# Optimization experiments

Hardware: AMD Instinct MI355X
Metric: run time of the kernel (lower is better)

The kernel has to match this reference:

```python
import jax, jax.numpy as jnp
import numpy as np

B, S, D, H = 4, 1024, 1024, 16
HD = D // H  # per-head dim = 64
NEG = -10000000000.0


def setup_inputs() -> dict:
    key = jax.random.key(0)
    ks = jax.random.split(key, 12)
    q = jax.random.normal(ks[0], (B, S, D), jnp.float32)
    k = jax.random.normal(ks[1], (B, S, D), jnp.float32)
    v = jax.random.normal(ks[2], (B, S, D), jnp.float32)
    mask = jax.random.randint(ks[3], (B, S, S), 0, 2).astype(jnp.int32)
    sc = 1.0 / np.sqrt(D)
    Wq = jax.random.normal(ks[4], (H, D, HD), jnp.float32) * sc
    bq = jnp.zeros((H, HD), jnp.float32)
    Wk = jax.random.normal(ks[5], (H, D, HD), jnp.float32) * sc
    bk = jnp.zeros((H, HD), jnp.float32)
    Wv = jax.random.normal(ks[6], (H, D, HD), jnp.float32) * sc
    bv = jnp.zeros((H, HD), jnp.float32)
    Wo = jax.random.normal(ks[7], (D, D), jnp.float32) * sc
    bo = jnp.zeros((D,), jnp.float32)
    return {"query": q, "key": k, "value": v, "attention_mask": mask,
            "Wq": Wq, "bq": bq, "Wk": Wk, "bk": bk, "Wv": Wv, "bv": bv,
            "Wo": Wo, "bo": bo}


def reference(query, key, value, attention_mask, Wq, bq, Wk, bk, Wv, bv, Wo, bo):
    # batched per-head projections: [B,S,D] x [H,D,E] -> [B,H,S,E]
    q = jnp.einsum('bsd,hde->bhse', query, Wq) + bq[None, :, None, :]
    k = jnp.einsum('bsd,hde->bhse', key, Wk) + bk[None, :, None, :]
    v = jnp.einsum('bsd,hde->bhse', value, Wv) + bv[None, :, None, :]
    # NOTE: scale uses key_dim (model_size = full D), faithful to source
    score = jnp.einsum('bhse,bhte->bhst', q, k) / jnp.sqrt(jnp.float32(D))
    m = attention_mask.astype(jnp.float32)[:, None, :, :]  # [B,1,S,S]
    score = score + (1.0 - m) * NEG
    attn = jax.nn.softmax(score, axis=-1) * m  # double masking
    heads = jnp.einsum('bhst,bhte->bhse', attn, v)  # [B,H,S,E]
    # concat heads along feature dim (head order preserved)
    heads = heads.transpose(0, 2, 1, 3).reshape(B, S, D)
    return heads @ Wo + bo
```

## Files before the change

kernel.cpp:

```cpp
#include <hip/hip_runtime.h>

#define B_ 4
#define S_ 1024
#define D_ 1024
#define H_ 16
#define E_ 64
#define BS_ (B_*S_)
#define BHSE_ (B_*H_*S_*E_)

typedef __attribute__((ext_vector_type(8))) short bf16x8;
typedef __attribute__((ext_vector_type(4))) float f32x4;

__device__ __forceinline__ unsigned short f2bf(float f) {
    unsigned int x = __float_as_uint(f);
    x = (x + 0x7FFFu + ((x >> 16) & 1u)) >> 16;
    return (unsigned short)x;
}
__device__ __forceinline__ float bf2f(unsigned short u) {
    return __uint_as_float(((unsigned int)u) << 16);
}
__device__ __forceinline__ float ldin(const void* p, size_t i, int isb) {
    return isb ? bf2f(((const unsigned short*)p)[i]) : ((const float*)p)[i];
}

#if __has_builtin(__builtin_amdgcn_exp2f)
#define EXP2(x) __builtin_amdgcn_exp2f(x)
#else
#define EXP2(x) __expf((x) * 0.6931471805599453f)
#endif

__device__ __forceinline__ void gl2lds16(const void* g, void* l) {
    __builtin_amdgcn_global_load_lds(
        (const __attribute__((address_space(1))) void*)g,
        (__attribute__((address_space(3))) void*)l, 16, 0, 0);
}

__global__ void detect_dtype(const unsigned int* q, int* flag) {
    __shared__ int cnt;
    if (threadIdx.x == 0) cnt = 0;
    __syncthreads();
    unsigned int w = q[threadIdx.x];
    unsigned int lo = w & 0xFFFFu;
    unsigned int e = (lo >> 7) & 0xFFu;
    int ok = (lo == 0u) || (e >= 100u && e <= 145u);
    atomicAdd(&cnt, ok);
    __syncthreads();
    if (threadIdx.x == 0) flag[0] = (cnt >= 240) ? 1 : 0;
}

__global__ __launch_bounds__(256) void conv_w2(
        const void* Wq, const void* Wk, const void* Wv, const void* Wo,
        const void* bq_, const void* bk_, const void* bv_, const void* bo_,
        unsigned short* WT, float* biases, const int* flag) {
    __shared__ unsigned short Tt[64][72];
    const int isb = flag[0];
    const int z = blockIdx.z, t = threadIdx.x;
    const void* src = (z == 0) ? Wq : (z == 1) ? Wk : (z == 2) ? Wv : Wo;
    const int r0 = blockIdx.y * 64;
    const int c0 = blockIdx.x;
    {
        int dl = t >> 2, qc = t & 3;
        size_t base;
        if (z < 3) base = (size_t)c0 * 65536 + (size_t)(r0 + dl) * 64 + qc * 16;
        else       base = (size_t)(r0 + dl) * 1024 + (size_t)c0 * 64 + qc * 16;
        if (isb) {
            const unsigned short* s = (const unsigned short*)src + base;
            bf16x8 a0 = *(const bf16x8*)s, a1 = *(const bf16x8*)(s + 8);
#pragma unroll
            for (int j = 0; j < 8; j++) {
                Tt[qc * 16 + j][dl] = (unsigned short)a0[j];
                Tt[qc * 16 + 8 + j][dl] = (unsigned short)a1[j];
            }
        } else {
            const float* s = (const float*)src + base;
#pragma unroll
            for (int j = 0; j < 16; j++) Tt[qc * 16 + j][dl] = f2bf(s[j]);
        }
    }
    __syncthreads();
    {
        int el = t >> 2, qc = t & 3;
        size_t dst = (size_t)z * D_ * D_ + (size_t)(c0 * 64 + el) * D_ + r0 + qc * 16;
        *(bf16x8*)&WT[dst]     = *(const bf16x8*)&Tt[el][qc * 16];
        *(bf16x8*)&WT[dst + 8] = *(const bf16x8*)&Tt[el][qc * 16 + 8];
    }
    if (z == 3 && blockIdx.y == 0 && blockIdx.x < 4) {
        const void* bs = (blockIdx.x == 0) ? bq_ : (blockIdx.x == 1) ? bk_
                       : (blockIdx.x == 2) ? bv_ : bo_;
#pragma unroll
        for (int j = 0; j < 4; j++) {
            int i = t * 4 + j;
            biases[blockIdx.x * 1024 + i] = ldin(bs, i, isb);
        }
    }
}

__global__ void maskpack(const int* mask, unsigned long long* packT) {
    int W = blockIdx.x * 4 + (threadIdx.x >> 6);
    int lane = threadIdx.x & 63;
    int b = W >> 14, rem = W & 16383, s = rem >> 4, kt = rem & 15;
    int mv = mask[((size_t)b * 1024 + s) * 1024 + kt * 64 + lane];
    unsigned long long bits = __ballot(mv != 0);
    if (lane == 0) packT[((size_t)b * 16 + kt) * 1024 + s] = bits;
}

__global__ __launch_bounds__(256) void conv_a(
        const float* q, const float* k, const float* v,
        unsigned short* dst, const int* flag) {
    if (flag[0]) return;
    const int z = blockIdx.x >> 11;
    const float* s = (z == 0) ? q : (z == 1) ? k : v;
    const size_t i = ((size_t)(blockIdx.x & 2047) * 256 + threadIdx.x) * 8;
    f32x4 a0 = *(const f32x4*)(s + i);
    f32x4 a1 = *(const f32x4*)(s + i + 4);
    bf16x8 o;
#pragma unroll
    for (int j = 0; j < 4; j++) {
        o[j]     = (short)f2bf(a0[j]);
        o[4 + j] = (short)f2bf(a1[j]);
    }
    *(bf16x8*)&dst[(size_t)z * ((size_t)BS_ * D_) + i] = o;
}

template<int BM, int BN, int MODE, int MINW>
__global__ __launch_bounds__(256, MINW) void gemm_k(
        const void* A0, const void* A1, const void* A2, const unsigned short* Aconv,
        const unsigned short* BtB, const float* biasB, void* dstB, const int* flag) {
    constexpr int TOT16 = (BM + BN) * 32;
    constexpr int CALLS = TOT16 / 512;
    constexpr int CPW = CALLS / 4;
    constexpr int MT = BM / 32;
    constexpr int NT = BN / 32;
    __shared__ unsigned short buf[2][TOT16];

    const int t = threadIdx.x, lane = t & 63, w = t >> 6;
    const int lm = lane & 15, q4 = lane >> 4;
    const int wm = w >> 1, wn = w & 1;
    const int lr = lane >> 2;
    const int ls = lane & 3;
    const int lg = ls ^ ((lr >> 1) & 3);
    const int fl = flag[0];

    const unsigned short* Abf;
    const unsigned short* Bt;
    const float* bias;
    int z = 0, m0, n0, phase;
    if (MODE == 0) {
        int bid = blockIdx.x + (blockIdx.y << 5) + (blockIdx.z << 9);
        int xcd = bid & 7, idx = bid >> 3;
        z = idx >> 6;
        int r = idx & 63;
        int mt = (xcd << 2) + (r & 3);
        int nt = r >> 2;
        m0 = mt * BM; n0 = nt * BN;
        phase = (nt * 13 + z * 5) & 31;
        const void* Ain = (z == 0) ? A0 : (z == 1 ? A1 : A2);
        Abf = fl ? (const unsigned short*)Ain
                 : Aconv + (size_t)z * ((size_t)BS_ * D_);
        Bt = BtB + (size_t)z * D_ * D_;
        bias = biasB + z * 1024;
    } else {
        Abf = (const unsigned short*)A0;
        Bt = BtB; bias = biasB;
        m0 = blockIdx.x * BM; n0 = blockIdx.y * BN;
        phase = (blockIdx.x * 7 + blockIdx.y * 13) & 31;
    }

    auto stage = [&](int kk, int bi) {
#pragma unroll
        for (int i = 0; i < CPW; ++i) {
            int c = w * CPW + i;
            int row = c * 16 + lr;
            const unsigned short* g;
            if (row < BM)
                g = Abf + (size_t)(m0 + row) * D_ + kk + lg * 8;
            else
                g = Bt + (size_t)(n0 + row - BM) * D_ + kk + lg * 8;
            gl2lds16(g, &buf[bi][c * 512]);
        }
    };

    f32x4 acc[MT][NT];
#pragma unroll
    for (int i = 0; i < MT; i++)
#pragma unroll
        for (int j = 0; j < NT; j++) acc[i][j] = (f32x4){0.f, 0.f, 0.f, 0.f};

    stage((phase & 31) * 32, 0);
    for (int it = 0; it < D_ / 32; ++it) {
        const int bi = it & 1;
        __syncthreads();
        if (it < D_ / 32 - 1) stage(((it + 1 + phase) & 31) * 32, bi ^ 1);

        const unsigned short* As = buf[bi];
        const unsigned short* Bs = buf[bi] + BM * 32;
        bf16x8 af[MT], bv[NT];
#pragma unroll
        for (int mt = 0; mt < MT; mt++) {
            int row = wm * (BM / 2) + mt * 16 + lm;
            af[mt] = *(const bf16x8*)&As[row * 32 + (q4 ^ ((row >> 1) & 3)) * 8];
        }
#pragma unroll
        for (int nt = 0; nt < NT; nt++) {
            int row = wn * (BN / 2) + nt * 16 + lm;
            bv[nt] = *(const bf16x8*)&Bs[row * 32 + (q4 ^ ((row >> 1) & 3)) * 8];
        }
#pragma unroll
        for (int mt = 0; mt < MT; mt++)
#pragma unroll
            for (int nt = 0; nt < NT; nt++)
                acc[mt][nt] = __builtin_amdgcn_mfma_f32_16x16x32_bf16(
                    af[mt], bv[nt], acc[mt][nt], 0, 0, 0);
    }

#pragma unroll
    for (int mt = 0; mt < MT; mt++)
#pragma unroll
        for (int nt = 0; nt < NT; nt++) {
            int N = n0 + wn * (BN / 2) + nt * 16 + lm;
            int Mb = m0 + wm * (BM / 2) + mt * 16 + q4 * 4;
            if (MODE == 0 && z == 2) {
                int bb = Mb >> 10, sb = Mb & 1023, hh = N >> 6, e = N & 63;
                unsigned long long hv = 0;
#pragma unroll
                for (int r = 0; r < 4; r++)
                    hv |= (unsigned long long)f2bf(acc[mt][nt][r] + bias[N]) << (16 * r);
                unsigned short* d16 = (unsigned short*)dstB + (size_t)2 * BHSE_;
                *(unsigned long long*)&d16[(((size_t)(bb * H_ + hh) * E_ + e) << 10) + sb] = hv;
            } else {
#pragma unroll
                for (int r = 0; r < 4; r++) {
                    int M = Mb + r;
                    float v = acc[mt][nt][r] + bias[N];
                    if (MODE == 0) {
                        int bb = M >> 10, s = M & 1023, hh = N >> 6, e = N & 63;
                        unsigned short* d16 = (unsigned short*)dstB + (size_t)z * BHSE_;
                        d16[((size_t)(bb * H_ + hh) * S_ + s) * E_ + e] = f2bf(v);
                    } else {
                        size_t idx = (size_t)M * D_ + N;
                        if (fl) ((unsigned short*)dstB)[idx] = f2bf(v);
                        else    ((float*)dstB)[idx] = v;
                    }
                }
            }
        }
}

#define PSTR 88
__global__ __launch_bounds__(256) void attn64(
        const unsigned short* Qp, const unsigned short* Kp, const unsigned short* VpT,
        const unsigned long long* packT, unsigned short* heads) {
    __shared__ unsigned short KT[2][4096];
    __shared__ unsigned short VT[2][4096];
    __shared__ unsigned short Pw[4][16 * PSTR];

    const int qt = blockIdx.x, h = blockIdx.y, b = blockIdx.z;
    const int t = threadIdx.x, w = t >> 6, lane = t & 63, lm = lane & 15, q4 = lane >> 4;
    const size_t bh = ((size_t)b * H_ + h) * S_ * E_;
    const unsigned short* Qb = Qp + bh;
    const unsigned short* Kb = Kp + bh;
    const unsigned short* Vb = VpT + bh;
    const int q0 = qt * 64 + w * 16;
    unsigned short* P = &Pw[w][0];

    const int l3 = lane >> 3, l7 = lane & 7;
    const int kLaneOff = l3 * 64 + (l7 ^ l3) * 8;
    const int vLaneOff = l3 * 1024 + (l7 ^ l3) * 8;

    const int sw = lm & 7;
    const int c0 = (q4 ^ sw) * 8, c1 = ((q4 ^ 4) ^ sw) * 8;

    bf16x8 bq0 = *(const bf16x8*)&Qb[(size_t)(q0 + lm) * E_ + q4 * 8];
    bf16x8 bq1 = *(const bf16x8*)&Qb[(size_t)(q0 + lm) * E_ + 32 + q4 * 8];

    f32x4 oacc[4];
#pragma unroll
    for (int i = 0; i < 4; i++) oacc[i] = (f32x4){0.f, 0.f, 0.f, 0.f};
    float mrun = -3.0e38f, lrun = 0.f;
    const float scale2 = 0.03125f * 1.4426950408889634f;

#define STAGE(ktile, bufi)                                                    \
    {                                                                         \
        int k0s = (ktile) * 64;                                               \
        _Pragma("unroll")                                                     \
        for (int i_ = 0; i_ < 4; ++i_) {                                      \
            int c_ = w * 4 + i_;                                              \
            if (c_ < 8) {                                                     \
                gl2lds16(Kb + (size_t)k0s * 64 + c_ * 512 + kLaneOff,         \
                         &KT[bufi][c_ * 512]);                                \
            } else {                                                          \
                int cc_ = c_ - 8;                                             \
                gl2lds16(Vb + (size_t)cc_ * 8192 + k0s + vLaneOff,            \
                         &VT[bufi][cc_ * 512]);                               \
            }                                                                 \
        }                                                                     \
    }

    STAGE(0, 0)

    for (int kt = 0; kt < S_ / 64; ++kt) {
        const int bufi = kt & 1;
        __syncthreads();
        if (kt < 15) STAGE(kt + 1, bufi ^ 1)

        unsigned long long mk = packT[((size_t)b * 16 + kt) * 1024 + q0 + lm];

        f32x4 st[4];
#pragma unroll
        for (int jt = 0; jt < 4; ++jt) {
            const unsigned short* kr = &KT[bufi][(jt * 16 + lm) * 64];
            bf16x8 ka0 = *(const bf16x8*)&kr[c0];
            bf16x8 ka1 = *(const bf16x8*)&kr[c1];
            f32x4 zz = (f32x4){0.f, 0.f, 0.f, 0.f};
            zz = __builtin_amdgcn_mfma_f32_16x16x32_bf16(ka0, bq0, zz, 0, 0, 0);
            zz = __builtin_amdgcn_mfma_f32_16x16x32_bf16(ka1, bq1, zz, 0, 0, 0);
            st[jt] = zz;
        }
        float sv[4][4];
        float tmx = -3.0e38f;
#pragma unroll
        for (int jt = 0; jt < 4; ++jt)
#pragma unroll
            for (int r = 0; r < 4; r++) {
                int kb = jt * 16 + q4 * 4 + r;
                float xm = ((mk >> kb) & 1ull) ? st[jt][r] * scale2 : -3.0e38f;
                sv[jt][r] = xm;
                tmx = fmaxf(tmx, xm);
            }
        tmx = fmaxf(tmx, __shfl_xor(tmx, 16, 64));
        tmx = fmaxf(tmx, __shfl_xor(tmx, 32, 64));
        float mnew = fmaxf(mrun, tmx);
        float alpha = EXP2(mrun - mnew);
        float ssum = 0.f;
        unsigned long long pk[4];
#pragma unroll
        for (int jt = 0; jt < 4; ++jt) {
            float p0 = EXP2(sv[jt][0] - mnew);
            float p1 = EXP2(sv[jt][1] - mnew);
            float p2 = EXP2(sv[jt][2] - mnew);
            float p3 = EXP2(sv[jt][3] - mnew);
            ssum += (p0 + p1) + (p2 + p3);
            pk[jt] = (unsigned long long)f2bf(p0)
                   | ((unsigned long long)f2bf(p1) << 16)
                   | ((unsigned long long)f2bf(p2) << 32)
                   | ((unsigned long long)f2bf(p3) << 48);
        }
        ssum += __shfl_xor(ssum, 16, 64);
        ssum += __shfl_xor(ssum, 32, 64);
        lrun = lrun * alpha + ssum;
        mrun = mnew;
#pragma unroll
        for (int nt = 0; nt < 4; nt++) oacc[nt] = oacc[nt] * alpha;

#pragma unroll
        for (int jt = 0; jt < 4; ++jt)
            *(unsigned long long*)&P[lm * PSTR + jt * 16 + q4 * 4] = pk[jt];
        bf16x8 bp0 = *(const bf16x8*)&P[lm * PSTR + q4 * 8];
        bf16x8 bp1 = *(const bf16x8*)&P[lm * PSTR + 32 + q4 * 8];

#pragma unroll
        for (int nt = 0; nt < 4; nt++) {
            const unsigned short* vr = &VT[bufi][(nt * 16 + lm) * 64];
            bf16x8 va0 = *(const bf16x8*)&vr[c0];
            bf16x8 va1 = *(const bf16x8*)&vr[c1];
            oacc[nt] = __builtin_amdgcn_mfma_f32_16x16x32_bf16(va0, bp0, oacc[nt], 0, 0, 0);
            oacc[nt] = __builtin_amdgcn_mfma_f32_16x16x32_bf16(va1, bp1, oacc[nt], 0, 0, 0);
        }
    }

    float inv = 1.0f / lrun;
#pragma unroll
    for (int nt = 0; nt < 4; nt++) {
        unsigned long long hv =
              (unsigned long long)f2bf(oacc[nt][0] * inv)
            | ((unsigned long long)f2bf(oacc[nt][1] * inv) << 16)
            | ((unsigned long long)f2bf(oacc[nt][2] * inv) << 32)
            | ((unsigned long long)f2bf(oacc[nt][3] * inv) << 48);
        *(unsigned long long*)&heads[(size_t)(b * S_ + q0 + lm) * D_ + h * E_ + nt * 16 + q4 * 4] = hv;
    }
}

extern "C" void kernel_launch(void* const* d_in, const int* in_sizes, int n_in,
                              void* d_out, int out_size, void* d_ws, size_t ws_size,
                              hipStream_t stream) {
    char* ws = (char*)d_ws;
    int* flag = (int*)ws;
    unsigned short* WT = (unsigned short*)(ws + 256);
    unsigned short* WqT = WT;
    unsigned short* WoT = WT + (size_t)3 * D_ * D_;
    float* biases = (float*)(WT + (size_t)4 * D_ * D_);
    float* bq = biases;
    float* bo = biases + 3 * 1024;
    unsigned short* Qp = (unsigned short*)(biases + 4 * 1024);
    unsigned short* Kp = Qp + (size_t)BHSE_;
    unsigned short* Vp = Kp + (size_t)BHSE_;
    unsigned short* heads = Vp + (size_t)BHSE_;
    unsigned long long* packT = (unsigned long long*)(heads + (size_t)BHSE_);
    unsigned short* Aconv = (unsigned short*)(packT + (size_t)B_ * 16 * S_);

    detect_dtype<<<1, 256, 0, stream>>>((const unsigned int*)d_in[0], flag);
    conv_w2<<<dim3(16, 16, 4), 256, 0, stream>>>(
        d_in[4], d_in[6], d_in[8], d_in[10],
        d_in[5], d_in[7], d_in[9], d_in[11], WT, biases, flag);
    maskpack<<<16384, 256, 0, stream>>>((const int*)d_in[3], packT);
    conv_a<<<6144, 256, 0, stream>>>(
        (const float*)d_in[0], (const float*)d_in[1], (const float*)d_in[2],
        Aconv, flag);
    gemm_k<128, 64, 0, 4><<<dim3(32, 16, 3), 256, 0, stream>>>(
        d_in[0], d_in[1], d_in[2], Aconv, WqT, bq, Qp, flag);
    attn64<<<dim3(16, 16, 4), 256, 0, stream>>>(Qp, Kp, Vp, packT, heads);
    gemm_k<64, 64, 1, 8><<<dim3(64, 16, 1), 256, 0, stream>>>(
        heads, nullptr, nullptr, nullptr, WoT, bo, d_out, flag);
}
```

Baseline: 261.1 us.

## Rework attention softmax: lazy rescale, hardware bf16 pack, bpermute P transpose

Reworks the online-softmax inner loop of the attention kernel. The running max is only updated when the new tile max exceeds it by more than a threshold, which skips most alpha rescales. Masking now zeroes probabilities after exp instead of selecting before it. Manual bf16 rounding is replaced by v_cvt_pk_bf16_f32, and the LDS round-trip for P is replaced by ds_bpermute shuffles, which frees the P shared buffer. Launch bounds now request 5 blocks per CU to raise occupancy. The lazy max risks numeric overflow only beyond the threshold, and the mask ignores max computation over masked entries, which may loosen the max estimate.

Result: faster. 251.7 us (-3.6%).

```diff
diff --git a/kernel.cpp b/kernel.cpp
--- a/kernel.cpp
+++ b/kernel.cpp
@@ -10,6 +10,7 @@
 
 typedef __attribute__((ext_vector_type(8))) short bf16x8;
 typedef __attribute__((ext_vector_type(4))) float f32x4;
+typedef __attribute__((ext_vector_type(4))) unsigned int u32x4;
 
 __device__ __forceinline__ unsigned short f2bf(float f) {
     unsigned int x = __float_as_uint(f);
@@ -21,6 +22,18 @@
 }
 __device__ __forceinline__ float ldin(const void* p, size_t i, int isb) {
     return isb ? bf2f(((const unsigned short*)p)[i]) : ((const float*)p)[i];
+}
+
+__device__ __forceinline__ unsigned int cvtpk(float lo, float hi) {
+    unsigned int r;
+    asm("v_cvt_pk_bf16_f32 %0, %1, %2" : "=v"(r) : "v"(lo), "v"(hi));
+    return r;
+}
+__device__ __forceinline__ unsigned int bperm(int srclane4, unsigned int v) {
+    return (unsigned int)__builtin_amdgcn_ds_bpermute(srclane4, (int)v);
+}
+__device__ __forceinline__ bf16x8 u4bf(u32x4 w) {
+    union { u32x4 u; bf16x8 h; } c; c.u = w; return c.h;
 }
 
 #if __has_builtin(__builtin_amdgcn_exp2f)
@@ -246,13 +259,11 @@
         }
 }
 
-#define PSTR 88
-__global__ __launch_bounds__(256) void attn64(
+__global__ __launch_bounds__(256, 5) void attn64(
         const unsigned short* Qp, const unsigned short* Kp, const unsigned short* VpT,
         const unsigned long long* packT, unsigned short* heads) {
     __shared__ unsigned short KT[2][4096];
     __shared__ unsigned short VT[2][4096];
-    __shared__ unsigned short Pw[4][16 * PSTR];
 
     const int qt = blockIdx.x, h = blockIdx.y, b = blockIdx.z;
     const int t = threadIdx.x, w = t >> 6, lane = t & 63, lm = lane & 15, q4 = lane >> 4;
@@ -261,7 +272,6 @@
     const unsigned short* Kb = Kp + bh;
     const unsigned short* Vb = VpT + bh;
     const int q0 = qt * 64 + w * 16;
-    unsigned short* P = &Pw[w][0];
 
     const int l3 = lane >> 3, l7 = lane & 7;
     const int kLaneOff = l3 * 64 + (l7 ^ l3) * 8;
@@ -269,6 +279,10 @@
 
     const int sw = lm & 7;
     const int c0 = (q4 ^ sw) * 8, c1 = ((q4 ^ 4) ^ sw) * 8;
+
+    const int srcA4 = ((lane & 15) | ((lane & 16) << 1)) << 2;
+    const int srcB4 = srcA4 + 64;
+    const bool selHi = (lane & 32) != 0;
 
     bf16x8 bq0 = *(const bf16x8*)&Qb[(size_t)(q0 + lm) * E_ + q4 * 8];
     bf16x8 bq1 = *(const bf16x8*)&Qb[(size_t)(q0 + lm) * E_ + 32 + q4 * 8];
@@ -316,47 +330,68 @@
             zz = __builtin_amdgcn_mfma_f32_16x16x32_bf16(ka1, bq1, zz, 0, 0, 0);
             st[jt] = zz;
         }
-        float sv[4][4];
+
         float tmx = -3.0e38f;
 #pragma unroll
         for (int jt = 0; jt < 4; ++jt)
 #pragma unroll
-            for (int r = 0; r < 4; r++) {
-                int kb = jt * 16 + q4 * 4 + r;
-                float xm = ((mk >> kb) & 1ull) ? st[jt][r] * scale2 : -3.0e38f;
-                sv[jt][r] = xm;
-                tmx = fmaxf(tmx, xm);
-            }
+            for (int r = 0; r < 4; r++) tmx = fmaxf(tmx, st[jt][r]);
         tmx = fmaxf(tmx, __shfl_xor(tmx, 16, 64));
         tmx = fmaxf(tmx, __shfl_xor(tmx, 32, 64));
-        float mnew = fmaxf(mrun, tmx);
-        float alpha = EXP2(mrun - mnew);
+        float pmax = tmx * scale2;
+
+        if (!__all(pmax - mrun <= 8.f)) {
+            float mnew = fmaxf(mrun, pmax);
+            float alpha = EXP2(mrun - mnew);
+            lrun *= alpha;
+#pragma unroll
+            for (int nt = 0; nt < 4; nt++) oacc[nt] = oacc[nt] * alpha;
+            mrun = mnew;
+        }
+        const float mneg = -mrun;
+
+        unsigned int mn = (unsigned int)(mk >> (q4 * 4));
+        unsigned int mh = (unsigned int)(mk >> (q4 * 4 + 32));
+
         float ssum = 0.f;
-        unsigned long long pk[4];
+        unsigned int cl[8];
 #pragma unroll
         for (int jt = 0; jt < 4; ++jt) {
-            float p0 = EXP2(sv[jt][0] - mnew);
-            float p1 = EXP2(sv[jt][1] - mnew);
-            float p2 = EXP2(sv[jt][2] - mnew);
-            float p3 = EXP2(sv[jt][3] - mnew);
+            unsigned int mm = (jt & 2) ? mh : mn;
+            const int sh = (jt & 1) * 16;
+            float p0 = EXP2(fmaf(st[jt][0], scale2, mneg));
+            float p1 = EXP2(fmaf(st[jt][1], scale2, mneg));
+            float p2 = EXP2(fmaf(st[jt][2], scale2, mneg));
+            float p3 = EXP2(fmaf(st[jt][3], scale2, mneg));
+            p0 = (mm & (1u << (sh + 0))) ? p0 : 0.f;
+            p1 = (mm & (1u << (sh + 1))) ? p1 : 0.f;
+            p2 = (mm & (1u << (sh + 2))) ? p2 : 0.f;
+            p3 = (mm & (1u << (sh + 3))) ? p3 : 0.f;
             ssum += (p0 + p1) + (p2 + p3);
-            pk[jt] = (unsigned long long)f2bf(p0)
-                   | ((unsigned long long)f2bf(p1) << 16)
-                   | ((unsigned long long)f2bf(p2) << 32)
-                   | ((unsigned long long)f2bf(p3) << 48);
+            cl[jt * 2]     = cvtpk(p0, p1);
+            cl[jt * 2 + 1] = cvtpk(p2, p3);
         }
         ssum += __shfl_xor(ssum, 16, 64);
         ssum += __shfl_xor(ssum, 32, 64);
-        lrun = lrun * alpha + ssum;
-        mrun = mnew;
-#pragma unroll
-        for (int nt = 0; nt < 4; nt++) oacc[nt] = oacc[nt] * alpha;
-
-#pragma unroll
-        for (int jt = 0; jt < 4; ++jt)
-            *(unsigned long long*)&P[lm * PSTR + jt * 16 + q4 * 4] = pk[jt];
-        bf16x8 bp0 = *(const bf16x8*)&P[lm * PSTR + q4 * 8];
-        bf16x8 bp1 = *(const bf16x8*)&P[lm * PSTR + 32 + q4 * 8];
+        lrun += ssum;
+
+        u32x4 w0, w1;
+        {
+            unsigned int aA0 = bperm(srcA4, cl[0]), aA2 = bperm(srcA4, cl[2]);
+            unsigned int aA1 = bperm(srcA4, cl[1]), aA3 = bperm(srcA4, cl[3]);
+            unsigned int aB0 = bperm(srcB4, cl[0]), aB2 = bperm(srcB4, cl[2]);
+            unsigned int aB1 = bperm(srcB4, cl[1]), aB3 = bperm(srcB4, cl[3]);
+            w0 = (u32x4){selHi ? aA2 : aA0, selHi ? aA3 : aA1,
+                         selHi ? aB2 : aB0, selHi ? aB3 : aB1};
+            unsigned int bA0 = bperm(srcA4, cl[4]), bA2 = bperm(srcA4, cl[6]);
+            unsigned int bA1 = bperm(srcA4, cl[5]), bA3 = bperm(srcA4, cl[7]);
+            unsigned int bB0 = bperm(srcB4, cl[4]), bB2 = bperm(srcB4, cl[6]);
+            unsigned int bB1 = bperm(srcB4, cl[5]), bB3 = bperm(srcB4, cl[7]);
+            w1 = (u32x4){selHi ? bA2 : bA0, selHi ? bA3 : bA1,
+                         selHi ? bB2 : bB0, selHi ? bB3 : bB1};
+        }
+        bf16x8 bp0 = u4bf(w0);
+        bf16x8 bp1 = u4bf(w1);
 
 #pragma unroll
         for (int nt = 0; nt < 4; nt++) {
@@ -371,11 +406,9 @@
     float inv = 1.0f / lrun;
 #pragma unroll
     for (int nt = 0; nt < 4; nt++) {
-        unsigned long long hv =
-              (unsigned long long)f2bf(oacc[nt][0] * inv)
-            | ((unsigned long long)f2bf(oacc[nt][1] * inv) << 16)
-            | ((unsigned long long)f2bf(oacc[nt][2] * inv) << 32)
-            | ((unsigned long long)f2bf(oacc[nt][3] * inv) << 48);
+        unsigned int lo = cvtpk(oacc[nt][0] * inv, oacc[nt][1] * inv);
+        unsigned int hi = cvtpk(oacc[nt][2] * inv, oacc[nt][3] * inv);
+        unsigned long long hv = (unsigned long long)lo | ((unsigned long long)hi << 32);
         *(unsigned long long*)&heads[(size_t)(b * S_ + q0 + lm) * D_ + h * E_ + nt * 16 + q4 * 4] = hv;
     }
 }
```
